# Performance work log

Hardware: AMD Instinct MI355X
Metric: run time of the kernel (lower is better)

The kernel has to match this reference:

```python
import jax, jax.numpy as jnp
import numpy as np


def setup_inputs() -> dict:
    key = jax.random.key(0)
    k1, k2 = jax.random.split(key)
    N, K, D = 400000, 50, 256
    locF = jax.random.normal(k1, (N, 1, D), dtype=jnp.float32)
    Ck = jax.random.normal(k2, (1, K, D), dtype=jnp.float32)
    return {"locF": locF, "Ck": Ck}


def reference(locF, Ck):
    # locF: [N, 1, D], Ck: [1, k, D]
    x = locF[:, 0, :]            # [N, D]
    c = Ck[0]                    # [k, D]
    k, D = c.shape
    # mean squared distance: ((x - c)**2).mean(-1) expanded to avoid [N,k,D] intermediate
    x2 = jnp.sum(x * x, axis=1, keepdims=True)        # [N, 1]
    c2 = jnp.sum(c * c, axis=1)                       # [k]
    d2 = (x2 - 2.0 * (x @ c.T) + c2) / D              # [N, k]
    index = jnp.argmin(d2, axis=1)                    # [N]
    # single-pass scatter-add of sums and counts keyed by argmin
    sums = jax.ops.segment_sum(x, index, num_segments=k)   # [k, D]
    counts = jnp.zeros((k,), dtype=jnp.int32).at[index].add(1)
    Ck1 = sums[None]            # [1, k, D]  (matches torch.cat along dim=1 of [1,1,D] chunks)
    nItems = counts[None]       # [1, k]
    return Ck1, nItems
```

## Files before the change

### kernel.cpp

```cpp
#include <hip/hip_runtime.h>


typedef _Float16 f16x8 __attribute__((ext_vector_type(8)));
typedef float    f32x4 __attribute__((ext_vector_type(4)));
typedef float    f32x16 __attribute__((ext_vector_type(16)));
typedef int      i32x4 __attribute__((ext_vector_type(4)));
typedef unsigned int u32x4 __attribute__((ext_vector_type(4)));

constexpr int K = 50, KP = 64, D = 256, KD = K * D;
constexpr int BLK = 1024, GRID = 512, CH = 32;
constexpr int SST = 68;

#define VMCNT0 asm volatile("s_waitcnt vmcnt(0)" ::: "memory")
#define LGKM0  asm volatile("s_waitcnt lgkmcnt(0)" ::: "memory")
#define SBAR   { __builtin_amdgcn_sched_barrier(0); __builtin_amdgcn_s_barrier(); __builtin_amdgcn_sched_barrier(0); }

__global__ __launch_bounds__(BLK)
void k_fused(const float* __restrict__ x, const float* __restrict__ cc,
             float* __restrict__ partial, float* __restrict__ out,
             int N, int useAtomic) {
    __shared__ _Float16       sC[K * D];
    __shared__ unsigned short sxh[2][CH * D];
    __shared__ float          sS[32 * SST];
    __shared__ float          sc2[KP];
    __shared__ int            sidx[2][CH];
    __shared__ int            scnt[K];

    const int tid = threadIdx.x;
    for (int i = tid; i < K * D; i += BLK) sC[i] = (_Float16)0.f;
    if (tid < K) scnt[tid] = 0;
    __syncthreads();
    for (int i = tid; i < KD; i += BLK) {
        int r = i >> 8, col = i & 255, ch = col >> 3, wd = col & 7;
        sC[r * D + (((ch ^ (r & 7)) << 3) | wd)] = (_Float16)cc[i];
    }
    if (tid < KP) {
        float s = 0.f;
        if (tid < K) for (int q = 0; q < D; ++q) { float v = cc[tid * D + q]; s += v * v; }
        sc2[tid] = s;
    }
    __syncthreads();

    const int lane = tid & 63, ci = lane & 15, g = lane >> 4, w = tid >> 6;
    const int wA   = (w >= 14) ? (w - 14) : 0;
    const int ra   = lane & 31;
    const int dl   = lane >> 5;
    const int rakey = (ra & 7) ^ (((ra >> 3) & 1) << 2);
    const int cl32 = wA * 32 + (lane & 31);
    const int clkey = (lane & 31) & 7;
    const _Float16* cbp = &sC[(cl32 < K ? cl32 : K - 1) * D];
    const int bcol = w * 16 + ci, bc3 = bcol >> 3, bce = bcol & 7;

    const int nCh = N / CH;
    const int cpb = nCh / gridDim.x, rem = nCh % gridDim.x;
    const int bid = blockIdx.x;
    const int lo  = bid * cpb + (bid < rem ? bid : rem);
    const int cnt = cpb + (bid < rem ? 1 : 0);

    const float INF = 3.4e38f;
    const float c2A = (cl32 < K) ? sc2[cl32] : INF;

    const int srow = 2 * w + (lane >> 5);
    const int scol = (lane & 31);
    const int skey = (srow & 7) ^ (((srow >> 3) & 1) << 2);
    f32x4 rA = {0,0,0,0}, rB = {0,0,0,0};
#define ISSUE(t_) { const float* b_ = x + (size_t)(t_) * (CH * D) + srow * D + 8 * scol; \
    rA = *(const f32x4*)(b_); rB = *(const f32x4*)(b_ + 4); }
#define WSLOT(s_) { \
    f16x8 h_ = {(_Float16)rA[0], (_Float16)rA[1], (_Float16)rA[2], (_Float16)rA[3], \
                (_Float16)rB[0], (_Float16)rB[1], (_Float16)rB[2], (_Float16)rB[3]}; \
    *(f16x8*)(&sxh[s_][srow * D + ((scol ^ skey) << 3)]) = h_; }

    f32x4 bacc0 = {0,0,0,0}, bacc1 = {0,0,0,0}, bacc2 = {0,0,0,0}, bacc3 = {0,0,0,0};

    if (cnt > 0) { ISSUE(lo) VMCNT0; WSLOT(0) if (cnt > 1) ISSUE(lo + 1) }
    LGKM0; SBAR;

    for (int i = 0; i <= cnt; ++i) {
        if (w >= 14 && i < cnt) {
            const unsigned short* xb = &sxh[i & 1][0];
            f32x16 acc = {0,0,0,0,0,0,0,0,0,0,0,0,0,0,0,0};
#define A_KS(ks) { \
            const int c_ = (ks) * 2 + dl; \
            f16x8 a = *(const f16x8*)(&xb[ra * D + ((c_ ^ rakey) << 3)]); \
            f16x8 b = *(const f16x8*)(cbp + ((c_ ^ clkey) << 3)); \
            acc = __builtin_amdgcn_mfma_f32_32x32x16_f16(a, b, acc, 0, 0, 0); }
            A_KS(0) A_KS(1) A_KS(2) A_KS(3) A_KS(4) A_KS(5) A_KS(6) A_KS(7)
            A_KS(8) A_KS(9) A_KS(10) A_KS(11) A_KS(12) A_KS(13) A_KS(14) A_KS(15)
#undef A_KS
#define DUMP(r) { const int row_ = ((r) & 3) + 8 * ((r) >> 2) + 4 * dl; \
            sS[row_ * SST + cl32] = c2A - 2.f * acc[r]; }
            DUMP(0) DUMP(1) DUMP(2) DUMP(3) DUMP(4) DUMP(5) DUMP(6) DUMP(7)
            DUMP(8) DUMP(9) DUMP(10) DUMP(11) DUMP(12) DUMP(13) DUMP(14) DUMP(15)
#undef DUMP
        }

        if (i >= 1) {
            const unsigned short* xbh = &sxh[(i - 1) & 1][0];
            const int jb = (i - 1) & 1;
            i32x4 idA = *(const i32x4*)(&sidx[jb][8 * g]);
            i32x4 idB = *(const i32x4*)(&sidx[jb][8 * g + 4]);
            unsigned short v0, v1, v2, v3, v4, v5, v6, v7;
#define RDH(j) { const int p_ = 8 * g + (j); const int key_ = (j) ^ ((g & 1) << 2); \
            v##j = xbh[p_ * D + ((bc3 ^ key_) << 3) + bce]; }
            RDH(0) RDH(1) RDH(2) RDH(3) RDH(4) RDH(5) RDH(6) RDH(7)
#undef RDH
            unsigned int w0 = (unsigned int)v0 | ((unsigned int)v1 << 16);
            unsigned int w1 = (unsigned int)v2 | ((unsigned int)v3 << 16);
            unsigned int w2 = (unsigned int)v4 | ((unsigned int)v5 << 16);
            unsigned int w3 = (unsigned int)v6 | ((unsigned int)v7 << 16);
            u32x4 W = {w0, w1, w2, w3};
            f16x8 bfr = __builtin_bit_cast(f16x8, W);
#define BMT(M, ACC) { \
            const int cl_ = (M) * 16 + ci; \
            f16x8 a = {(_Float16)(idA[0] == cl_ ? 1.f : 0.f), (_Float16)(idA[1] == cl_ ? 1.f : 0.f), \
                       (_Float16)(idA[2] == cl_ ? 1.f : 0.f), (_Float16)(idA[3] == cl_ ? 1.f : 0.f), \
                       (_Float16)(idB[0] == cl_ ? 1.f : 0.f), (_Float16)(idB[1] == cl_ ? 1.f : 0.f), \
                       (_Float16)(idB[2] == cl_ ? 1.f : 0.f), (_Float16)(idB[3] == cl_ ? 1.f : 0.f)}; \
            ACC = __builtin_amdgcn_mfma_f32_16x16x32_f16(a, bfr, ACC, 0, 0, 0); }
            BMT(0, bacc0) BMT(1, bacc1) BMT(2, bacc2) BMT(3, bacc3)
#undef BMT
        }

        LGKM0; SBAR;

        if (i + 1 < cnt) {
            VMCNT0;
            WSLOT((i + 1) & 1)
            if (i + 2 < cnt) ISSUE(lo + i + 2)
        }

        if (w >= 8 && w < 10 && i < cnt) {
            const int p_ = (w - 8) * 16 + (lane & 15);
            const int kq = lane >> 4;
            const float* sp = &sS[p_ * SST + kq * 16];
            f32x4 s0 = *(const f32x4*)(sp);
            f32x4 s1 = *(const f32x4*)(sp + 4);
            f32x4 s2 = *(const f32x4*)(sp + 8);
            f32x4 s3 = *(const f32x4*)(sp + 12);
            float bm = s0[0]; int bb = kq * 16;
#define CMP(V, E, OFF) { float s_ = V[E]; int c_ = kq * 16 + (OFF); \
            if (s_ < bm) { bm = s_; bb = c_; } }
            CMP(s0,1,1) CMP(s0,2,2) CMP(s0,3,3)
            CMP(s1,0,4) CMP(s1,1,5) CMP(s1,2,6) CMP(s1,3,7)
            CMP(s2,0,8) CMP(s2,1,9) CMP(s2,2,10) CMP(s2,3,11)
            CMP(s3,0,12) CMP(s3,1,13) CMP(s3,2,14) CMP(s3,3,15)
#undef CMP
            { float pm = __shfl_xor(bm, 16, 64); int pb = __shfl_xor(bb, 16, 64);
              if (pm < bm || (pm == bm && pb < bb)) { bm = pm; bb = pb; } }
            { float pm = __shfl_xor(bm, 32, 64); int pb = __shfl_xor(bb, 32, 64);
              if (pm < bm || (pm == bm && pb < bb)) { bm = pm; bb = pb; } }
            if (kq == 0) { sidx[i & 1][p_] = bb; atomicAdd(&scnt[bb], 1); }
        }
        LGKM0; SBAR;
    }

    if (useAtomic) {
#define WBK(M, ACC) { \
        { int cl_ = (M)*16 + 4*g + 0; if (cl_ < K) atomicAdd(&out[cl_ * D + bcol], ACC[0]); } \
        { int cl_ = (M)*16 + 4*g + 1; if (cl_ < K) atomicAdd(&out[cl_ * D + bcol], ACC[1]); } \
        { int cl_ = (M)*16 + 4*g + 2; if (cl_ < K) atomicAdd(&out[cl_ * D + bcol], ACC[2]); } \
        { int cl_ = (M)*16 + 4*g + 3; if (cl_ < K) atomicAdd(&out[cl_ * D + bcol], ACC[3]); } }
        WBK(0, bacc0) WBK(1, bacc1) WBK(2, bacc2) WBK(3, bacc3)
#undef WBK
    } else {
        float* pb = partial + (size_t)bid * KD;
#define WBK(M, ACC) { \
        { int cl_ = (M)*16 + 4*g + 0; if (cl_ < K) pb[cl_ * D + bcol] = ACC[0]; } \
        { int cl_ = (M)*16 + 4*g + 1; if (cl_ < K) pb[cl_ * D + bcol] = ACC[1]; } \
        { int cl_ = (M)*16 + 4*g + 2; if (cl_ < K) pb[cl_ * D + bcol] = ACC[2]; } \
        { int cl_ = (M)*16 + 4*g + 3; if (cl_ < K) pb[cl_ * D + bcol] = ACC[3]; } }
        WBK(0, bacc0) WBK(1, bacc1) WBK(2, bacc2) WBK(3, bacc3)
#undef WBK
    }
    __syncthreads();
    for (int k = tid; k < K; k += BLK) atomicAdd(&out[KD + k], (float)scnt[k]);
}

__global__ __launch_bounds__(256)
void k_reduce(const float* __restrict__ partial, float* __restrict__ out, int G) {
    const int j  = blockIdx.x * 256 + threadIdx.x;
    const int bs = G / 8;
    const int b0 = blockIdx.y * bs;
    float s = 0.f;
    for (int b = b0; b < b0 + bs; ++b) s += partial[(size_t)b * KD + j];
    atomicAdd(&out[j], s);
}

extern "C" void kernel_launch(void* const* d_in, const int* in_sizes, int n_in,
                              void* d_out, int out_size, void* d_ws, size_t ws_size,
                              hipStream_t stream) {
    const float* x = (const float*)d_in[0];
    const float* c = (const float*)d_in[1];
    float* out = (float*)d_out;
    const int N = in_sizes[0] / D;

    float* partial = (float*)d_ws;
    const size_t need = (size_t)GRID * KD * sizeof(float);
    const int useAtomic = (ws_size < need) ? 1 : 0;

    hipMemsetAsync(d_out, 0, (size_t)out_size * sizeof(float), stream);
    k_fused<<<GRID, BLK, 0, stream>>>(x, c, partial, out, N, useAtomic);
    if (!useAtomic) {
        k_reduce<<<dim3(KD / 256, 8), 256, 0, stream>>>(partial, out, GRID);
    }
}
```

Baseline: 147.6 us.

## Split distance MFMA K-dimension across four waves and widen argmin to four waves

The distance GEMM previously ran on two waves, each doing all 16 k-steps. It now runs on four waves: waves 12-15 each cover half of D and write partial scores into two separate LDS buffers. The argmin stage now uses four waves, with eight lanes per row and a three-step shuffle reduction, and it sums the two partial buffers before comparing. This shortens the critical path of the per-chunk distance stage. In exchange it adds an extra LDS buffer, extra LDS reads, and more waves busy in that phase.

```diff
diff --git a/kernel.cpp b/kernel.cpp
--- a/kernel.cpp
+++ b/kernel.cpp
@@ -21,7 +21,8 @@
              int N, int useAtomic) {
     __shared__ _Float16       sC[K * D];
     __shared__ unsigned short sxh[2][CH * D];
-    __shared__ float          sS[32 * SST];
+    __shared__ float          sS0[32 * SST];
+    __shared__ float          sS1[32 * SST];
     __shared__ float          sc2[KP];
     __shared__ int            sidx[2][CH];
     __shared__ int            scnt[K];
@@ -42,7 +43,8 @@
     __syncthreads();
 
     const int lane = tid & 63, ci = lane & 15, g = lane >> 4, w = tid >> 6;
-    const int wA   = (w >= 14) ? (w - 14) : 0;
+    const int kh   = (w >= 14) ? 1 : 0;
+    const int wA   = w & 1;
     const int ra   = lane & 31;
     const int dl   = lane >> 5;
     const int rakey = (ra & 7) ^ (((ra >> 3) & 1) << 2);
@@ -77,22 +79,29 @@
     LGKM0; SBAR;
 
     for (int i = 0; i <= cnt; ++i) {
-        if (w >= 14 && i < cnt) {
+        if (w >= 12 && i < cnt) {
             const unsigned short* xb = &sxh[i & 1][0];
             f32x16 acc = {0,0,0,0,0,0,0,0,0,0,0,0,0,0,0,0};
-#define A_KS(ks) { \
-            const int c_ = (ks) * 2 + dl; \
+#define A_KS(s) { \
+            const int c_ = (kh * 8 + (s)) * 2 + dl; \
             f16x8 a = *(const f16x8*)(&xb[ra * D + ((c_ ^ rakey) << 3)]); \
             f16x8 b = *(const f16x8*)(cbp + ((c_ ^ clkey) << 3)); \
             acc = __builtin_amdgcn_mfma_f32_32x32x16_f16(a, b, acc, 0, 0, 0); }
             A_KS(0) A_KS(1) A_KS(2) A_KS(3) A_KS(4) A_KS(5) A_KS(6) A_KS(7)
-            A_KS(8) A_KS(9) A_KS(10) A_KS(11) A_KS(12) A_KS(13) A_KS(14) A_KS(15)
 #undef A_KS
+            if (kh == 0) {
 #define DUMP(r) { const int row_ = ((r) & 3) + 8 * ((r) >> 2) + 4 * dl; \
-            sS[row_ * SST + cl32] = c2A - 2.f * acc[r]; }
-            DUMP(0) DUMP(1) DUMP(2) DUMP(3) DUMP(4) DUMP(5) DUMP(6) DUMP(7)
-            DUMP(8) DUMP(9) DUMP(10) DUMP(11) DUMP(12) DUMP(13) DUMP(14) DUMP(15)
+                sS0[row_ * SST + cl32] = c2A - 2.f * acc[r]; }
+                DUMP(0) DUMP(1) DUMP(2) DUMP(3) DUMP(4) DUMP(5) DUMP(6) DUMP(7)
+                DUMP(8) DUMP(9) DUMP(10) DUMP(11) DUMP(12) DUMP(13) DUMP(14) DUMP(15)
 #undef DUMP
+            } else {
+#define DUMP(r) { const int row_ = ((r) & 3) + 8 * ((r) >> 2) + 4 * dl; \
+                sS1[row_ * SST + cl32] = -2.f * acc[r]; }
+                DUMP(0) DUMP(1) DUMP(2) DUMP(3) DUMP(4) DUMP(5) DUMP(6) DUMP(7)
+                DUMP(8) DUMP(9) DUMP(10) DUMP(11) DUMP(12) DUMP(13) DUMP(14) DUMP(15)
+#undef DUMP
+            }
         }
 
         if (i >= 1) {
@@ -130,27 +139,27 @@
             if (i + 2 < cnt) ISSUE(lo + i + 2)
         }
 
-        if (w >= 8 && w < 10 && i < cnt) {
-            const int p_ = (w - 8) * 16 + (lane & 15);
-            const int kq = lane >> 4;
-            const float* sp = &sS[p_ * SST + kq * 16];
-            f32x4 s0 = *(const f32x4*)(sp);
-            f32x4 s1 = *(const f32x4*)(sp + 4);
-            f32x4 s2 = *(const f32x4*)(sp + 8);
-            f32x4 s3 = *(const f32x4*)(sp + 12);
-            float bm = s0[0]; int bb = kq * 16;
-#define CMP(V, E, OFF) { float s_ = V[E]; int c_ = kq * 16 + (OFF); \
+        if (w >= 8 && w < 12 && i < cnt) {
+            const int p_ = (w - 8) * 8 + (lane >> 3);
+            const int q  = lane & 7;
+            const float* s0p = &sS0[p_ * SST + 8 * q];
+            const float* s1p = &sS1[p_ * SST + 8 * q];
+            f32x4 a0 = *(const f32x4*)(s0p), a1 = *(const f32x4*)(s0p + 4);
+            f32x4 b0 = *(const f32x4*)(s1p), b1 = *(const f32x4*)(s1p + 4);
+            f32x4 u = a0 + b0, v = a1 + b1;
+            float bm = u[0]; int bb = 8 * q;
+#define CMP(VV, E, OFF) { float s_ = VV[E]; int c_ = 8 * q + (OFF); \
             if (s_ < bm) { bm = s_; bb = c_; } }
-            CMP(s0,1,1) CMP(s0,2,2) CMP(s0,3,3)
-            CMP(s1,0,4) CMP(s1,1,5) CMP(s1,2,6) CMP(s1,3,7)
-            CMP(s2,0,8) CMP(s2,1,9) CMP(s2,2,10) CMP(s2,3,11)
-            CMP(s3,0,12) CMP(s3,1,13) CMP(s3,2,14) CMP(s3,3,15)
+            CMP(u,1,1) CMP(u,2,2) CMP(u,3,3)
+            CMP(v,0,4) CMP(v,1,5) CMP(v,2,6) CMP(v,3,7)
 #undef CMP
-            { float pm = __shfl_xor(bm, 16, 64); int pb = __shfl_xor(bb, 16, 64);
+            { float pm = __shfl_xor(bm, 1, 64); int pb = __shfl_xor(bb, 1, 64);
               if (pm < bm || (pm == bm && pb < bb)) { bm = pm; bb = pb; } }
-            { float pm = __shfl_xor(bm, 32, 64); int pb = __shfl_xor(bb, 32, 64);
+            { float pm = __shfl_xor(bm, 2, 64); int pb = __shfl_xor(bb, 2, 64);
               if (pm < bm || (pm == bm && pb < bb)) { bm = pm; bb = pb; } }
-            if (kq == 0) { sidx[i & 1][p_] = bb; atomicAdd(&scnt[bb], 1); }
+            { float pm = __shfl_xor(bm, 4, 64); int pb = __shfl_xor(bb, 4, 64);
+              if (pm < bm || (pm == bm && pb < bb)) { bm = pm; bb = pb; } }
+            if (q == 0) { sidx[i & 1][p_] = bb; atomicAdd(&scnt[bb], 1); }
         }
         LGKM0; SBAR;
     }
```

Result: faster. 136.7 us (-7.4%).
